# Kernel optimization log

Measured on AMD Instinct MI355X. Metric: run time of the kernel, lower is better.

The kernel has to match this reference:

```python
import jax, jax.numpy as jnp
import numpy as np

N = 100000   # nodes
E = 1600000  # edges
FEAT = 128
HID = 128
TGT = 64
L = 3
G = 512      # graphs in batch


def setup_inputs() -> dict:
    key = jax.random.key(0)
    ks = jax.random.split(key, 16)
    s = 0.05
    return {
        "x": jax.random.normal(ks[0], (N, FEAT), jnp.float32),
        "edge_index": jax.random.randint(ks[1], (2, E), 0, N, dtype=jnp.int32),
        "batch": jnp.sort(jax.random.randint(ks[2], (N,), 0, G, dtype=jnp.int32)),
        "conv_w1": jax.random.normal(ks[3], (L, FEAT, HID), jnp.float32) * s,
        "conv_b1": jax.random.normal(ks[4], (L, HID), jnp.float32) * s,
        "conv_w2": jax.random.normal(ks[5], (L, HID, HID), jnp.float32) * s,
        "conv_b2": jax.random.normal(ks[6], (L, HID), jnp.float32) * s,
        "eps": jnp.zeros((L,), jnp.float32),
        "gn_scale": jnp.ones((L, HID), jnp.float32),
        "gn_weight": jnp.ones((L, HID), jnp.float32),
        "gn_bias": jnp.zeros((L, HID), jnp.float32),
        "proj_w1": jax.random.normal(ks[7], (L, HID, HID), jnp.float32) * s,
        "proj_b1": jax.random.normal(ks[8], (L, HID), jnp.float32) * s,
        "proj_w2": jax.random.normal(ks[9], (L, HID, TGT), jnp.float32) * s,
        "proj_b2": jax.random.normal(ks[10], (L, TGT), jnp.float32) * s,
    }


def _graph_norm(h, batch, counts, scale, weight, bias):
    # per-graph mean -> scatter back to nodes
    mean = jax.ops.segment_sum(h, batch, num_segments=G) / counts
    sub = h - mean[batch] * scale
    var = jax.ops.segment_sum(sub * sub, batch, num_segments=G) / counts
    std = jnp.sqrt(var + 1e-8)
    return weight * sub / std[batch] + bias


def reference(x, edge_index, batch, conv_w1, conv_b1, conv_w2, conv_b2, eps,
              gn_scale, gn_weight, gn_bias, proj_w1, proj_b1, proj_w2, proj_b2):
    src, dst = edge_index[0], edge_index[1]
    counts = jnp.maximum(
        jax.ops.segment_sum(jnp.ones((N, 1), x.dtype), batch, num_segments=G), 1.0)
    h = x
    z_cat = []
    for l in range(L):
        # GINConv: aggr_j->i then 2-layer MLP
        aggr = jax.ops.segment_sum(h[src], dst, num_segments=N)
        h = (1.0 + eps[l]) * h + aggr
        h = jax.nn.relu(h @ conv_w1[l] + conv_b1[l]) @ conv_w2[l] + conv_b2[l]
        # GraphNorm
        h = _graph_norm(h, batch, counts, gn_scale[l], gn_weight[l], gn_bias[l])
        h = jax.nn.relu(h)
        # projection MLP + global add pool
        z = jax.nn.relu(h @ proj_w1[l] + proj_b1[l]) @ proj_w2[l] + proj_b2[l]
        z_cat.append(jax.ops.segment_sum(z, batch, num_segments=G))
    return jnp.concatenate(z_cat, axis=-1)  # [G, L*TGT]
```

## Files before the change

### kernel.cpp

```cpp
#include <hip/hip_runtime.h>

#define NN 100000
#define EE 1600000
#define HIDD 128
#define TGTT 64
#define GGG 512
#define NBK 98
#define CAPB 17408
#define ABLK 200
#define LSTR 136
#define CVTB 3125
#define GBLK 1563
#define FOUTB 128
#define OUTB 128

typedef unsigned short ushort_t;
typedef __attribute__((ext_vector_type(8))) short short8;
typedef __attribute__((ext_vector_type(4))) float f32x4;
typedef __attribute__((ext_vector_type(4))) unsigned short us4;

__device__ __forceinline__ float b2f(ushort_t u) {
    union { unsigned int i; float f; } v; v.i = ((unsigned int)u) << 16; return v.f;
}
__device__ __forceinline__ ushort_t f2b(float f) {
    union { float f; unsigned int i; } v; v.f = f;
    unsigned int r = (v.i + 0x7fffu + ((v.i >> 16) & 1u)) >> 16;
    return (ushort_t)r;
}

__global__ __launch_bounds__(256) void k_pro(const float* __restrict__ x, ushort_t* __restrict__ Xb,
                                             const float* __restrict__ cw1, const float* __restrict__ cw2,
                                             const float* __restrict__ pw1, ushort_t* __restrict__ Wt,
                                             const int* __restrict__ batch, int* __restrict__ goff,
                                             const int* __restrict__ ei, int* __restrict__ gcnt,
                                             unsigned int* __restrict__ bbuf) {
    __shared__ ushort_t sW[128 * 129];
    __shared__ int cnt[NBK], base[NBK], cur[NBK];
    int b = blockIdx.x, t = threadIdx.x;

    if (b < CVTB) {
        long i0 = (long)b * 1024 + t;
#pragma unroll
        for (int c = 0; c < 4; c++) {
            long i = i0 + c * 256;
            float4 v = ((const float4*)x)[i];
            us4 o; o.x = f2b(v.x); o.y = f2b(v.y); o.z = f2b(v.z); o.w = f2b(v.w);
            ((us4*)Xb)[i] = o;
        }
        return;
    }
    b -= CVTB;
    if (b < 9) {
        int l = b / 3, j = b % 3;
        const float* src = (j == 0 ? cw1 : j == 1 ? cw2 : pw1) + (size_t)l * HIDD * HIDD;
        ushort_t* dst = Wt + (size_t)b * HIDD * HIDD;
        for (int i = t; i < HIDD * HIDD; i += 256) {
            int k = i >> 7, n = i & 127;
            sW[n * 129 + k] = f2b(src[i]);
        }
        __syncthreads();
        for (int i = t; i < HIDD * HIDD; i += 256) {
            dst[i] = sW[(i >> 7) * 129 + (i & 127)];
        }
        return;
    }
    b -= 9;
    if (b < 3) {
        int g = b * 256 + t;
        if (g > GGG) return;
        int lo = 0, hi = NN;
        while (lo < hi) { int mid = (lo + hi) >> 1; if (batch[mid] < g) lo = mid + 1; else hi = mid; }
        goff[g] = lo;
        return;
    }
    b -= 3;
    {
        if (t < NBK) cnt[t] = 0;
        __syncthreads();
        int e0 = b * 8000;
        int e1 = min(e0 + 8000, EE);
        for (int e = e0 + t; e < e1; e += 256)
            atomicAdd(&cnt[ei[EE + e] >> 10], 1);
        __syncthreads();
        if (t < NBK) { base[t] = atomicAdd(&gcnt[t], cnt[t]); cur[t] = 0; }
        __syncthreads();
        for (int e = e0 + t; e < e1; e += 256) {
            int s = ei[e], d = ei[EE + e];
            int bk = d >> 10;
            int off = base[bk] + atomicAdd(&cur[bk], 1);
            if (off < CAPB)
                bbuf[(long)bk * CAPB + off] = (unsigned int)s | (((unsigned int)d & 1023u) << 17);
        }
    }
}

__global__ __launch_bounds__(256) void k_csr(const int* __restrict__ gcnt,
                                             const unsigned int* __restrict__ bbuf,
                                             int* __restrict__ rowptr, int* __restrict__ csr) {
    __shared__ int ldeg[1024], lcur[1024], tsum[256], sb[NBK];
    int b = blockIdx.x, t = threadIdx.x;
    if (t < NBK) sb[t] = gcnt[t];
    __syncthreads();
    if (t == 0) { int a = 0; for (int i = 0; i < NBK; i++) { int v = sb[i]; sb[i] = a; a += v; } }
    __syncthreads();
    int cnt = min(gcnt[b], CAPB);
    int base = sb[b];
    const unsigned int* bb = bbuf + (long)b * CAPB;
#pragma unroll
    for (int i = 0; i < 4; i++) ldeg[t + 256 * i] = 0;
    __syncthreads();
    for (int i = t; i < cnt; i += 256) atomicAdd(&ldeg[bb[i] >> 17], 1);
    __syncthreads();
    int d0 = ldeg[4 * t], d1 = ldeg[4 * t + 1], d2 = ldeg[4 * t + 2], d3 = ldeg[4 * t + 3];
    int tot = d0 + d1 + d2 + d3;
    tsum[t] = tot;
    __syncthreads();
    for (int off = 1; off < 256; off <<= 1) {
        int u = (t >= off) ? tsum[t - off] : 0;
        __syncthreads();
        tsum[t] += u;
        __syncthreads();
    }
    int texcl = tsum[t] - tot;
    int p0 = base + texcl, p1 = p0 + d0, p2 = p1 + d1, p3 = p2 + d2;
    lcur[4 * t] = p0; lcur[4 * t + 1] = p1; lcur[4 * t + 2] = p2; lcur[4 * t + 3] = p3;
    int gnode = b * 1024 + 4 * t;
    if (gnode < NN)     rowptr[gnode]     = p0;
    if (gnode + 1 < NN) rowptr[gnode + 1] = p1;
    if (gnode + 2 < NN) rowptr[gnode + 2] = p2;
    if (gnode + 3 < NN) rowptr[gnode + 3] = p3;
    if (b == NBK - 1 && t == 0) rowptr[NN] = EE;
    __syncthreads();
    for (int i = t; i < cnt; i += 256) {
        unsigned int en = bb[i];
        int pos = atomicAdd(&lcur[en >> 17], 1);
        csr[pos] = (int)(en & 0x1FFFFu);
    }
}

__global__ __launch_bounds__(256, 8) void k_gmlp(const ushort_t* __restrict__ hin,
                                              const int* __restrict__ rowptr,
                                              const int* __restrict__ csr,
                                              const float* __restrict__ eps, int l,
                                              const ushort_t* __restrict__ Wt1, const float* __restrict__ B1,
                                              const ushort_t* __restrict__ Wt2, const float* __restrict__ B2,
                                              ushort_t* __restrict__ Y,
                                              const float* __restrict__ pooledP, const int* __restrict__ goff,
                                              const float* __restrict__ WoP, const float* __restrict__ BoP,
                                              float* __restrict__ outP, int lprev) {
    __shared__ ushort_t sX[64 * LSTR];
    int tid = threadIdx.x;

    if (blockIdx.x >= GBLK) {
        if (lprev < 0) return;
        int ob = blockIdx.x - GBLK;
        int sub = tid >> 6, tt = tid & 63;
        int g = ob * 4 + sub;
        if (g >= GGG) return;
        float cntg = (float)(goff[g + 1] - goff[g]);
        float acc = cntg * BoP[tt];
        const float* p = pooledP + (long)g * HIDD;
        for (int k = 0; k < HIDD; k++) acc += p[k] * WoP[k * TGTT + tt];
        outP[(long)g * (3 * TGTT) + lprev * TGTT + tt] = acc;
        return;
    }

    long base = (long)blockIdx.x * 64;
    int lane = tid & 15, ng = tid >> 4;
    int off = lane << 3;
    float e1 = 1.0f + eps[l];

#pragma unroll 1
    for (int it = 0; it < 4; it++) {
        int row = it * 16 + ng;
        long node = base + row;
        short8 o = (short8)0;
        if (node < NN) {
            short8 h = *(const short8*)(hin + (node << 7) + off);
            float acc[8];
#pragma unroll
            for (int t = 0; t < 8; t++) acc[t] = e1 * b2f((ushort_t)h[t]);
            int jb = rowptr[node], je = rowptr[node + 1];
            int j = jb;
            for (; j + 8 <= je; j += 8) {
                int s0 = csr[j], s1 = csr[j + 1], s2 = csr[j + 2], s3 = csr[j + 3];
                int s4 = csr[j + 4], s5 = csr[j + 5], s6 = csr[j + 6], s7 = csr[j + 7];
                short8 v0 = *(const short8*)(hin + ((long)s0 << 7) + off);
                short8 v1 = *(const short8*)(hin + ((long)s1 << 7) + off);
                short8 v2 = *(const short8*)(hin + ((long)s2 << 7) + off);
                short8 v3 = *(const short8*)(hin + ((long)s3 << 7) + off);
                short8 v4 = *(const short8*)(hin + ((long)s4 << 7) + off);
                short8 v5 = *(const short8*)(hin + ((long)s5 << 7) + off);
                short8 v6 = *(const short8*)(hin + ((long)s6 << 7) + off);
                short8 v7 = *(const short8*)(hin + ((long)s7 << 7) + off);
#pragma unroll
                for (int t = 0; t < 8; t++)
                    acc[t] += ((b2f((ushort_t)v0[t]) + b2f((ushort_t)v1[t])) +
                               (b2f((ushort_t)v2[t]) + b2f((ushort_t)v3[t]))) +
                              ((b2f((ushort_t)v4[t]) + b2f((ushort_t)v5[t])) +
                               (b2f((ushort_t)v6[t]) + b2f((ushort_t)v7[t])));
            }
            for (; j + 4 <= je; j += 4) {
                int s0 = csr[j], s1 = csr[j + 1], s2 = csr[j + 2], s3 = csr[j + 3];
                short8 v0 = *(const short8*)(hin + ((long)s0 << 7) + off);
                short8 v1 = *(const short8*)(hin + ((long)s1 << 7) + off);
                short8 v2 = *(const short8*)(hin + ((long)s2 << 7) + off);
                short8 v3 = *(const short8*)(hin + ((long)s3 << 7) + off);
#pragma unroll
                for (int t = 0; t < 8; t++)
                    acc[t] += (b2f((ushort_t)v0[t]) + b2f((ushort_t)v1[t])) +
                              (b2f((ushort_t)v2[t]) + b2f((ushort_t)v3[t]));
            }
            for (; j < je; j++) {
                int s = csr[j];
                short8 v = *(const short8*)(hin + ((long)s << 7) + off);
#pragma unroll
                for (int t = 0; t < 8; t++) acc[t] += b2f((ushort_t)v[t]);
            }
#pragma unroll
            for (int t = 0; t < 8; t++) o[t] = (short)f2b(acc[t]);
        }
        *(short8*)(sX + row * LSTR + off) = o;
    }
    __syncthreads();

    int w = tid >> 6, l64 = tid & 63, q = l64 >> 4, l16 = l64 & 15;
    int r0 = w * 16;
    short8 a0[4];
#pragma unroll
    for (int c = 0; c < 4; c++)
        a0[c] = *(const short8*)(sX + (r0 + l16) * LSTR + q * 8 + c * 32);
    f32x4 acc0[8];
#pragma unroll
    for (int nt = 0; nt < 8; nt++) {
        int col = nt * 16 + l16;
        float bias = B1[col];
        f32x4 c0 = {bias, bias, bias, bias};
        const ushort_t* bB = Wt1 + col * HIDD + q * 8;
#pragma unroll
        for (int c = 0; c < 4; c++) {
            short8 b = *(const short8*)(bB + c * 32);
            c0 = __builtin_amdgcn_mfma_f32_16x16x32_bf16(a0[c], b, c0, 0, 0, 0);
        }
        acc0[nt] = c0;
    }
#pragma unroll
    for (int nt = 0; nt < 8; nt++) {
        int col = nt * 16 + l16;
#pragma unroll
        for (int r = 0; r < 4; r++)
            sX[(r0 + q * 4 + r) * LSTR + col] = f2b(fmaxf(acc0[nt][r], 0.f));
    }
#pragma unroll
    for (int c = 0; c < 4; c++)
        a0[c] = *(const short8*)(sX + (r0 + l16) * LSTR + q * 8 + c * 32);
#pragma unroll
    for (int nt = 0; nt < 8; nt++) {
        int col = nt * 16 + l16;
        float bias = B2[col];
        f32x4 c0 = {bias, bias, bias, bias};
        const ushort_t* bB = Wt2 + col * HIDD + q * 8;
#pragma unroll
        for (int c = 0; c < 4; c++) {
            short8 b = *(const short8*)(bB + c * 32);
            c0 = __builtin_amdgcn_mfma_f32_16x16x32_bf16(a0[c], b, c0, 0, 0, 0);
        }
#pragma unroll
        for (int r = 0; r < 4; r++) {
            long row0 = base + r0 + q * 4 + r;
            if (row0 < NN) Y[(row0 << 7) + col] = f2b(c0[r]);
        }
    }
}

__global__ __launch_bounds__(512) void k_gstat(const ushort_t* __restrict__ Hraw,
                                               const int* __restrict__ goff,
                                               const float* __restrict__ scale,
                                               const float* __restrict__ weight,
                                               float* __restrict__ msb, float* __restrict__ invb,
                                               float* __restrict__ pooled) {
    __shared__ float red[2][32][128];
    int g = blockIdx.x;
    int s = goff[g], e = goff[g + 1];
    float cnt = (float)max(e - s, 1);
    int lane = threadIdx.x & 15;
    int rg = threadIdx.x >> 4;
    int f0 = lane << 3;
    float sum[8], sq[8];
#pragma unroll
    for (int t = 0; t < 8; t++) { sum[t] = 0.f; sq[t] = 0.f; }
    for (int i = s + rg; i < e; i += 32) {
        short8 v = *(const short8*)(Hraw + ((long)i << 7) + f0);
#pragma unroll
        for (int t = 0; t < 8; t++) { float a = b2f((ushort_t)v[t]); sum[t] += a; sq[t] += a * a; }
    }
#pragma unroll
    for (int t = 0; t < 8; t++) { red[0][rg][f0 + t] = sum[t]; red[1][rg][f0 + t] = sq[t]; }
    __syncthreads();
    for (int off = 16; off > 0; off >>= 1) {
        if (rg < off) {
#pragma unroll
            for (int t = 0; t < 8; t++) {
                red[0][rg][f0 + t] += red[0][rg + off][f0 + t];
                red[1][rg][f0 + t] += red[1][rg + off][f0 + t];
            }
        }
        __syncthreads();
    }
    if (rg == 0) {
#pragma unroll
        for (int t = 0; t < 8; t++) {
            int f = f0 + t;
            float mean = red[0][0][f] / cnt;
            float ms = mean * scale[f];
            float var = red[1][0][f] / cnt - 2.f * ms * mean + ms * ms;
            msb[g * HIDD + f] = ms;
            invb[g * HIDD + f] = weight[f] / sqrtf(var + 1e-8f);
            pooled[g * HIDD + f] = 0.f;
        }
    }
}

__global__ __launch_bounds__(256, 8) void k_projpool(const ushort_t* __restrict__ Hraw,
                                                  const int* __restrict__ batch,
                                                  const float* __restrict__ msb, const float* __restrict__ invb,
                                                  const float* __restrict__ gnb,
                                                  const ushort_t* __restrict__ Wt, const float* __restrict__ B,
                                                  ushort_t* __restrict__ Hn, float* __restrict__ pooled,
                                                  int store_hn) {
    __shared__ ushort_t sX[64 * LSTR];
    __shared__ int sgid[64];
    int tid = threadIdx.x;
    long base = (long)blockIdx.x * 64;
#pragma unroll
    for (int c = 0; c < 4; c++) {
        int idx = c * 256 + tid;
        int row = idx >> 4, cw = idx & 15;
        long grow = base + row;
        short8 v = (short8)0;
        if (grow < NN) {
            short8 raw = *(const short8*)(Hraw + (grow << 7) + (cw << 3));
            int g = batch[grow];
            if (cw == 0) sgid[row] = g;
            const float* msp = msb + g * HIDD + (cw << 3);
            const float* ivp = invb + g * HIDD + (cw << 3);
            const float* gbp = gnb + (cw << 3);
            float4 m0 = *(const float4*)msp, m1 = *(const float4*)(msp + 4);
            float4 i0 = *(const float4*)ivp, i1 = *(const float4*)(ivp + 4);
            float4 g0 = *(const float4*)gbp, g1 = *(const float4*)(gbp + 4);
            float mv[8] = {m0.x, m0.y, m0.z, m0.w, m1.x, m1.y, m1.z, m1.w};
            float iv[8] = {i0.x, i0.y, i0.z, i0.w, i1.x, i1.y, i1.z, i1.w};
            float gv[8] = {g0.x, g0.y, g0.z, g0.w, g1.x, g1.y, g1.z, g1.w};
#pragma unroll
            for (int t = 0; t < 8; t++) {
                float val = (b2f((ushort_t)raw[t]) - mv[t]) * iv[t] + gv[t];
                v[t] = (short)f2b(val > 0.f ? val : 0.f);
            }
            if (store_hn) *(short8*)(Hn + (grow << 7) + (cw << 3)) = v;
        } else if (cw == 0) {
            sgid[row] = -1;
        }
        *(short8*)(sX + row * LSTR + (cw << 3)) = v;
    }
    __syncthreads();

    int w = tid >> 6, l64 = tid & 63, q = l64 >> 4, l16 = l64 & 15;
    int r0 = w * 16;
    short8 a0[4];
#pragma unroll
    for (int c = 0; c < 4; c++)
        a0[c] = *(const short8*)(sX + (r0 + l16) * LSTR + q * 8 + c * 32);
    f32x4 acc0[8];
#pragma unroll
    for (int nt = 0; nt < 8; nt++) {
        int col = nt * 16 + l16;
        float bias = B[col];
        f32x4 c0 = {bias, bias, bias, bias};
        const ushort_t* bB = Wt + col * HIDD + q * 8;
#pragma unroll
        for (int c = 0; c < 4; c++) {
            short8 b = *(const short8*)(bB + c * 32);
            c0 = __builtin_amdgcn_mfma_f32_16x16x32_bf16(a0[c], b, c0, 0, 0, 0);
        }
        acc0[nt] = c0;
    }
#pragma unroll
    for (int nt = 0; nt < 8; nt++) {
        int col = nt * 16 + l16;
#pragma unroll
        for (int r = 0; r < 4; r++)
            sX[(r0 + q * 4 + r) * LSTR + col] = f2b(fmaxf(acc0[nt][r], 0.f));
    }
    __syncthreads();

    int f = tid & 127, half = tid >> 7;
    int rbeg = half * 32, rend = rbeg + 32;
    float sum = 0.f;
    int curg = -1;
    for (int row = rbeg; row < rend; row++) {
        int g = sgid[row];
        if (g != curg) {
            if (curg >= 0) atomicAdd(&pooled[(long)curg * HIDD + f], sum);
            sum = 0.f; curg = g;
        }
        if (g >= 0) sum += b2f(sX[row * LSTR + f]);
    }
    if (curg >= 0) atomicAdd(&pooled[(long)curg * HIDD + f], sum);
}

__global__ __launch_bounds__(256) void k_out(const float* __restrict__ pooled, const int* __restrict__ goff,
                                             const float* __restrict__ W, const float* __restrict__ B,
                                             float* __restrict__ out, int l) {
    int sub = threadIdx.x >> 6, tt = threadIdx.x & 63;
    int g = blockIdx.x * 4 + sub;
    if (g >= GGG) return;
    float cnt = (float)(goff[g + 1] - goff[g]);
    float acc = cnt * B[tt];
    const float* p = pooled + (long)g * HIDD;
    for (int k = 0; k < HIDD; k++) acc += p[k] * W[k * TGTT + tt];
    out[(long)g * (3 * TGTT) + l * TGTT + tt] = acc;
}

extern "C" void kernel_launch(void* const* d_in, const int* in_sizes, int n_in,
                              void* d_out, int out_size, void* d_ws, size_t ws_size,
                              hipStream_t stream) {
    const float* x    = (const float*)d_in[0];
    const int*   ei   = (const int*)d_in[1];
    const int*   batch= (const int*)d_in[2];
    const float* cw1  = (const float*)d_in[3];
    const float* cb1  = (const float*)d_in[4];
    const float* cw2  = (const float*)d_in[5];
    const float* cb2  = (const float*)d_in[6];
    const float* eps  = (const float*)d_in[7];
    const float* gsc  = (const float*)d_in[8];
    const float* gw   = (const float*)d_in[9];
    const float* gb   = (const float*)d_in[10];
    const float* pw1  = (const float*)d_in[11];
    const float* pb1  = (const float*)d_in[12];
    const float* pw2  = (const float*)d_in[13];
    const float* pb2  = (const float*)d_in[14];
    float* out = (float*)d_out;

    ushort_t* Xb   = (ushort_t*)d_ws;
    ushort_t* Hn   = Xb;
    ushort_t* Hraw = Xb + (size_t)NN * HIDD;
    ushort_t* Wt   = Hraw + (size_t)NN * HIDD;
    float* msb     = (float*)(Wt + (size_t)9 * HIDD * HIDD);
    float* invb    = msb + (size_t)GGG * HIDD;
    float* pooled  = invb + (size_t)GGG * HIDD;
    int* goff   = (int*)(pooled + (size_t)GGG * HIDD);
    int* rowptr = goff + (GGG + 1);
    int* gcnt   = rowptr + (NN + 1);
    int* csr    = gcnt + NBK;
    unsigned int* bbuf = (unsigned int*)(csr + EE);

    hipMemsetAsync(gcnt, 0, NBK * sizeof(int), stream);
    k_pro<<<CVTB + 9 + 3 + ABLK, 256, 0, stream>>>(x, Xb, cw1, cw2, pw1, Wt, batch, goff, ei, gcnt, bbuf);
    k_csr<<<NBK, 256, 0, stream>>>(gcnt, bbuf, rowptr, csr);

    for (int l = 0; l < 3; l++) {
        const ushort_t* hin = (l == 0) ? Xb : Hn;
        ushort_t* Wt1 = Wt + (size_t)(l * 3 + 0) * HIDD * HIDD;
        ushort_t* Wt2 = Wt + (size_t)(l * 3 + 1) * HIDD * HIDD;
        ushort_t* Wtp = Wt + (size_t)(l * 3 + 2) * HIDD * HIDD;
        int grid = GBLK + (l > 0 ? FOUTB : 0);
        k_gmlp<<<grid, 256, 0, stream>>>(hin, rowptr, csr, eps, l,
                                         Wt1, cb1 + l * HIDD, Wt2, cb2 + l * HIDD, Hraw,
                                         pooled, goff,
                                         pw2 + (size_t)(l - 1) * HIDD * TGTT, pb2 + (l - 1) * TGTT,
                                         out, l - 1);
        k_gstat<<<GGG, 512, 0, stream>>>(Hraw, goff, gsc + l * HIDD, gw + l * HIDD, msb, invb, pooled);
        k_projpool<<<GBLK, 256, 0, stream>>>(Hraw, batch, msb, invb, gb + l * HIDD,
                                             Wtp, pb1 + l * HIDD, Hn, pooled, (l < 2) ? 1 : 0);
    }
    k_out<<<OUTB, 256, 0, stream>>>(pooled, goff, pw2 + (size_t)2 * HIDD * TGTT, pb2 + 2 * TGTT, out, 2);
}
```

Measured before the change: 676.4 us.

## Restructure preprocessing, CSR build, projection pooling, and output stage

After: 660.2 us. 1.02x faster.

```diff
diff --git a/kernel.cpp b/kernel.cpp
--- a/kernel.cpp
+++ b/kernel.cpp
@@ -7,12 +7,12 @@
 #define GGG 512
 #define NBK 98
 #define CAPB 17408
-#define ABLK 200
+#define ABLK 800
+#define EPB 2000
+#define CVT2 512
 #define LSTR 136
-#define CVTB 3125
-#define GBLK 1563
-#define FOUTB 128
-#define OUTB 128
+#define GBLKG 1563
+#define GBLKP 782
 
 typedef unsigned short ushort_t;
 typedef __attribute__((ext_vector_type(8))) short short8;
@@ -34,51 +34,14 @@
                                              const int* __restrict__ batch, int* __restrict__ goff,
                                              const int* __restrict__ ei, int* __restrict__ gcnt,
                                              unsigned int* __restrict__ bbuf) {
-    __shared__ ushort_t sW[128 * 129];
     __shared__ int cnt[NBK], base[NBK], cur[NBK];
     int b = blockIdx.x, t = threadIdx.x;
 
-    if (b < CVTB) {
-        long i0 = (long)b * 1024 + t;
-#pragma unroll
-        for (int c = 0; c < 4; c++) {
-            long i = i0 + c * 256;
-            float4 v = ((const float4*)x)[i];
-            us4 o; o.x = f2b(v.x); o.y = f2b(v.y); o.z = f2b(v.z); o.w = f2b(v.w);
-            ((us4*)Xb)[i] = o;
-        }
-        return;
-    }
-    b -= CVTB;
-    if (b < 9) {
-        int l = b / 3, j = b % 3;
-        const float* src = (j == 0 ? cw1 : j == 1 ? cw2 : pw1) + (size_t)l * HIDD * HIDD;
-        ushort_t* dst = Wt + (size_t)b * HIDD * HIDD;
-        for (int i = t; i < HIDD * HIDD; i += 256) {
-            int k = i >> 7, n = i & 127;
-            sW[n * 129 + k] = f2b(src[i]);
-        }
-        __syncthreads();
-        for (int i = t; i < HIDD * HIDD; i += 256) {
-            dst[i] = sW[(i >> 7) * 129 + (i & 127)];
-        }
-        return;
-    }
-    b -= 9;
-    if (b < 3) {
-        int g = b * 256 + t;
-        if (g > GGG) return;
-        int lo = 0, hi = NN;
-        while (lo < hi) { int mid = (lo + hi) >> 1; if (batch[mid] < g) lo = mid + 1; else hi = mid; }
-        goff[g] = lo;
-        return;
-    }
-    b -= 3;
-    {
+    if (b < ABLK) {
         if (t < NBK) cnt[t] = 0;
         __syncthreads();
-        int e0 = b * 8000;
-        int e1 = min(e0 + 8000, EE);
+        int e0 = b * EPB;
+        int e1 = min(e0 + EPB, EE);
         for (int e = e0 + t; e < e1; e += 256)
             atomicAdd(&cnt[ei[EE + e] >> 10], 1);
         __syncthreads();
@@ -91,80 +54,84 @@
             if (off < CAPB)
                 bbuf[(long)bk * CAPB + off] = (unsigned int)s | (((unsigned int)d & 1023u) << 17);
         }
-    }
-}
-
-__global__ __launch_bounds__(256) void k_csr(const int* __restrict__ gcnt,
-                                             const unsigned int* __restrict__ bbuf,
-                                             int* __restrict__ rowptr, int* __restrict__ csr) {
-    __shared__ int ldeg[1024], lcur[1024], tsum[256], sb[NBK];
+        return;
+    }
+    b -= ABLK;
+    if (b < CVT2) {
+        long total = (long)NN * HIDD / 4;
+        long step = (long)CVT2 * 256;
+        for (long i = (long)b * 256 + t; i < total; i += step) {
+            float4 v = ((const float4*)x)[i];
+            us4 o; o.x = f2b(v.x); o.y = f2b(v.y); o.z = f2b(v.z); o.w = f2b(v.w);
+            ((us4*)Xb)[i] = o;
+        }
+        return;
+    }
+    b -= CVT2;
+    if (b < 9) {
+        int l = b / 3, j = b % 3;
+        const float* src = (j == 0 ? cw1 : j == 1 ? cw2 : pw1) + (size_t)l * HIDD * HIDD;
+        ushort_t* dst = Wt + (size_t)b * HIDD * HIDD;
+        for (int i = t; i < HIDD * HIDD; i += 256)
+            dst[(i & 127) * HIDD + (i >> 7)] = f2b(src[i]);
+        return;
+    }
+    b -= 9;
+    {
+        int g = b * 256 + t;
+        if (g > GGG) return;
+        int lo = 0, hi = NN;
+        while (lo < hi) { int mid = (lo + hi) >> 1; if (batch[mid] < g) lo = mid + 1; else hi = mid; }
+        goff[g] = lo;
+    }
+}
+
+__global__ __launch_bounds__(1024) void k_csr(const int* __restrict__ gcnt,
+                                              const unsigned int* __restrict__ bbuf,
+                                              int* __restrict__ rowptr, int* __restrict__ csr) {
+    __shared__ int ldeg[1024], tsum[1024], sb[NBK];
     int b = blockIdx.x, t = threadIdx.x;
     if (t < NBK) sb[t] = gcnt[t];
+    ldeg[t] = 0;
     __syncthreads();
     if (t == 0) { int a = 0; for (int i = 0; i < NBK; i++) { int v = sb[i]; sb[i] = a; a += v; } }
     __syncthreads();
     int cnt = min(gcnt[b], CAPB);
     int base = sb[b];
     const unsigned int* bb = bbuf + (long)b * CAPB;
-#pragma unroll
-    for (int i = 0; i < 4; i++) ldeg[t + 256 * i] = 0;
-    __syncthreads();
-    for (int i = t; i < cnt; i += 256) atomicAdd(&ldeg[bb[i] >> 17], 1);
-    __syncthreads();
-    int d0 = ldeg[4 * t], d1 = ldeg[4 * t + 1], d2 = ldeg[4 * t + 2], d3 = ldeg[4 * t + 3];
-    int tot = d0 + d1 + d2 + d3;
-    tsum[t] = tot;
-    __syncthreads();
-    for (int off = 1; off < 256; off <<= 1) {
+    for (int i = t; i < cnt; i += 1024) atomicAdd(&ldeg[bb[i] >> 17], 1);
+    __syncthreads();
+    int d0 = ldeg[t];
+    tsum[t] = d0;
+    __syncthreads();
+    for (int off = 1; off < 1024; off <<= 1) {
         int u = (t >= off) ? tsum[t - off] : 0;
         __syncthreads();
         tsum[t] += u;
         __syncthreads();
     }
-    int texcl = tsum[t] - tot;
-    int p0 = base + texcl, p1 = p0 + d0, p2 = p1 + d1, p3 = p2 + d2;
-    lcur[4 * t] = p0; lcur[4 * t + 1] = p1; lcur[4 * t + 2] = p2; lcur[4 * t + 3] = p3;
-    int gnode = b * 1024 + 4 * t;
-    if (gnode < NN)     rowptr[gnode]     = p0;
-    if (gnode + 1 < NN) rowptr[gnode + 1] = p1;
-    if (gnode + 2 < NN) rowptr[gnode + 2] = p2;
-    if (gnode + 3 < NN) rowptr[gnode + 3] = p3;
+    int p0 = base + tsum[t] - d0;
+    int gnode = b * 1024 + t;
+    if (gnode < NN) rowptr[gnode] = p0;
     if (b == NBK - 1 && t == 0) rowptr[NN] = EE;
-    __syncthreads();
-    for (int i = t; i < cnt; i += 256) {
+    ldeg[t] = p0;
+    __syncthreads();
+    for (int i = t; i < cnt; i += 1024) {
         unsigned int en = bb[i];
-        int pos = atomicAdd(&lcur[en >> 17], 1);
+        int pos = atomicAdd(&ldeg[en >> 17], 1);
         csr[pos] = (int)(en & 0x1FFFFu);
     }
 }
 
-__global__ __launch_bounds__(256, 8) void k_gmlp(const ushort_t* __restrict__ hin,
+__global__ __launch_bounds__(256) void k_gmlp(const ushort_t* __restrict__ hin,
                                               const int* __restrict__ rowptr,
                                               const int* __restrict__ csr,
                                               const float* __restrict__ eps, int l,
                                               const ushort_t* __restrict__ Wt1, const float* __restrict__ B1,
                                               const ushort_t* __restrict__ Wt2, const float* __restrict__ B2,
-                                              ushort_t* __restrict__ Y,
-                                              const float* __restrict__ pooledP, const int* __restrict__ goff,
-                                              const float* __restrict__ WoP, const float* __restrict__ BoP,
-                                              float* __restrict__ outP, int lprev) {
+                                              ushort_t* __restrict__ Y) {
     __shared__ ushort_t sX[64 * LSTR];
     int tid = threadIdx.x;
-
-    if (blockIdx.x >= GBLK) {
-        if (lprev < 0) return;
-        int ob = blockIdx.x - GBLK;
-        int sub = tid >> 6, tt = tid & 63;
-        int g = ob * 4 + sub;
-        if (g >= GGG) return;
-        float cntg = (float)(goff[g + 1] - goff[g]);
-        float acc = cntg * BoP[tt];
-        const float* p = pooledP + (long)g * HIDD;
-        for (int k = 0; k < HIDD; k++) acc += p[k] * WoP[k * TGTT + tt];
-        outP[(long)g * (3 * TGTT) + lprev * TGTT + tt] = acc;
-        return;
-    }
-
     long base = (long)blockIdx.x * 64;
     int lane = tid & 15, ng = tid >> 4;
     int off = lane << 3;
@@ -266,10 +233,18 @@
             c0 = __builtin_amdgcn_mfma_f32_16x16x32_bf16(a0[c], b, c0, 0, 0, 0);
         }
 #pragma unroll
-        for (int r = 0; r < 4; r++) {
-            long row0 = base + r0 + q * 4 + r;
-            if (row0 < NN) Y[(row0 << 7) + col] = f2b(c0[r]);
-        }
+        for (int r = 0; r < 4; r++)
+            sX[(r0 + q * 4 + r) * LSTR + col] = f2b(c0[r]);
+    }
+    __syncthreads();
+
+#pragma unroll
+    for (int c = 0; c < 4; c++) {
+        int idx = c * 256 + tid;
+        int row = idx >> 4, cw = idx & 15;
+        long grow = base + row;
+        if (grow < NN)
+            *(short8*)(Y + (grow << 7) + (cw << 3)) = *(const short8*)(sX + row * LSTR + (cw << 3));
     }
 }
 
@@ -277,8 +252,7 @@
                                                const int* __restrict__ goff,
                                                const float* __restrict__ scale,
                                                const float* __restrict__ weight,
-                                               float* __restrict__ msb, float* __restrict__ invb,
-                                               float* __restrict__ pooled) {
+                                               float* __restrict__ msb, float* __restrict__ invb) {
     __shared__ float red[2][32][128];
     int g = blockIdx.x;
     int s = goff[g], e = goff[g + 1];
@@ -316,24 +290,23 @@
             float var = red[1][0][f] / cnt - 2.f * ms * mean + ms * ms;
             msb[g * HIDD + f] = ms;
             invb[g * HIDD + f] = weight[f] / sqrtf(var + 1e-8f);
-            pooled[g * HIDD + f] = 0.f;
-        }
-    }
-}
-
-__global__ __launch_bounds__(256, 8) void k_projpool(const ushort_t* __restrict__ Hraw,
+        }
+    }
+}
+
+__global__ __launch_bounds__(256) void k_projpool(const ushort_t* __restrict__ Hraw,
                                                   const int* __restrict__ batch,
                                                   const float* __restrict__ msb, const float* __restrict__ invb,
                                                   const float* __restrict__ gnb,
                                                   const ushort_t* __restrict__ Wt, const float* __restrict__ B,
-                                                  ushort_t* __restrict__ Hn, float* __restrict__ pooled,
+                                                  ushort_t* __restrict__ Hn, float* __restrict__ partial,
                                                   int store_hn) {
-    __shared__ ushort_t sX[64 * LSTR];
-    __shared__ int sgid[64];
+    __shared__ ushort_t sX[128 * LSTR];
+    __shared__ int sgid[128];
     int tid = threadIdx.x;
-    long base = (long)blockIdx.x * 64;
-#pragma unroll
-    for (int c = 0; c < 4; c++) {
+    long base = (long)blockIdx.x * 128;
+#pragma unroll
+    for (int c = 0; c < 8; c++) {
         int idx = c * 256 + tid;
         int row = idx >> 4, cw = idx & 15;
         long grow = base + row;
@@ -365,60 +338,88 @@
     __syncthreads();
 
     int w = tid >> 6, l64 = tid & 63, q = l64 >> 4, l16 = l64 & 15;
-    int r0 = w * 16;
-    short8 a0[4];
-#pragma unroll
-    for (int c = 0; c < 4; c++)
+    int r0 = w * 16, r1 = 64 + w * 16;
+    short8 a0[4], a1[4];
+#pragma unroll
+    for (int c = 0; c < 4; c++) {
         a0[c] = *(const short8*)(sX + (r0 + l16) * LSTR + q * 8 + c * 32);
-    f32x4 acc0[8];
+        a1[c] = *(const short8*)(sX + (r1 + l16) * LSTR + q * 8 + c * 32);
+    }
+    f32x4 acc0[8], acc1[8];
 #pragma unroll
     for (int nt = 0; nt < 8; nt++) {
         int col = nt * 16 + l16;
         float bias = B[col];
         f32x4 c0 = {bias, bias, bias, bias};
+        f32x4 c1 = c0;
         const ushort_t* bB = Wt + col * HIDD + q * 8;
 #pragma unroll
         for (int c = 0; c < 4; c++) {
             short8 b = *(const short8*)(bB + c * 32);
             c0 = __builtin_amdgcn_mfma_f32_16x16x32_bf16(a0[c], b, c0, 0, 0, 0);
-        }
-        acc0[nt] = c0;
+            c1 = __builtin_amdgcn_mfma_f32_16x16x32_bf16(a1[c], b, c1, 0, 0, 0);
+        }
+        acc0[nt] = c0; acc1[nt] = c1;
     }
 #pragma unroll
     for (int nt = 0; nt < 8; nt++) {
         int col = nt * 16 + l16;
 #pragma unroll
-        for (int r = 0; r < 4; r++)
+        for (int r = 0; r < 4; r++) {
             sX[(r0 + q * 4 + r) * LSTR + col] = f2b(fmaxf(acc0[nt][r], 0.f));
+            sX[(r1 + q * 4 + r) * LSTR + col] = f2b(fmaxf(acc1[nt][r], 0.f));
+        }
     }
     __syncthreads();
 
     int f = tid & 127, half = tid >> 7;
-    int rbeg = half * 32, rend = rbeg + 32;
+    int g0 = sgid[0];
+    long pbase = ((long)blockIdx.x * 4) * 2 + half;
+#pragma unroll
+    for (int s = 0; s < 4; s++)
+        partial[(pbase + (long)s * 2) * 128 + f] = 0.f;
+    int rbeg = half * 64, rend = rbeg + 64;
     float sum = 0.f;
     int curg = -1;
     for (int row = rbeg; row < rend; row++) {
         int g = sgid[row];
         if (g != curg) {
-            if (curg >= 0) atomicAdd(&pooled[(long)curg * HIDD + f], sum);
+            if (curg >= 0) partial[(pbase + (long)(curg - g0) * 2) * 128 + f] = sum;
             sum = 0.f; curg = g;
         }
         if (g >= 0) sum += b2f(sX[row * LSTR + f]);
     }
-    if (curg >= 0) atomicAdd(&pooled[(long)curg * HIDD + f], sum);
-}
-
-__global__ __launch_bounds__(256) void k_out(const float* __restrict__ pooled, const int* __restrict__ goff,
-                                             const float* __restrict__ W, const float* __restrict__ B,
-                                             float* __restrict__ out, int l) {
-    int sub = threadIdx.x >> 6, tt = threadIdx.x & 63;
-    int g = blockIdx.x * 4 + sub;
-    if (g >= GGG) return;
-    float cnt = (float)(goff[g + 1] - goff[g]);
-    float acc = cnt * B[tt];
-    const float* p = pooled + (long)g * HIDD;
-    for (int k = 0; k < HIDD; k++) acc += p[k] * W[k * TGTT + tt];
-    out[(long)g * (3 * TGTT) + l * TGTT + tt] = acc;
+    if (curg >= 0) partial[(pbase + (long)(curg - g0) * 2) * 128 + f] = sum;
+}
+
+__global__ __launch_bounds__(128) void k_poolred(const float* __restrict__ partial,
+                                                 const int* __restrict__ batch,
+                                                 const int* __restrict__ goff,
+                                                 const float* __restrict__ W, const float* __restrict__ B,
+                                                 float* __restrict__ out, int l) {
+    __shared__ float pv[128];
+    int g = blockIdx.x, f = threadIdx.x;
+    int s0 = goff[g], e0 = goff[g + 1];
+    float sum = 0.f;
+    if (e0 > s0) {
+        int bs = s0 >> 7, be = (e0 - 1) >> 7;
+        for (int b = bs; b <= be; b++) {
+            int g0 = batch[(long)b << 7];
+            int s = g - g0;
+            if (s >= 0 && s < 4) {
+                long pbase = ((long)b * 4 + s) * 2;
+                sum += partial[pbase * 128 + f] + partial[(pbase + 1) * 128 + f];
+            }
+        }
+    }
+    pv[f] = sum;
+    __syncthreads();
+    if (f < TGTT) {
+        float cnt = (float)(e0 - s0);
+        float acc = cnt * B[f];
+        for (int k = 0; k < HIDD; k++) acc += pv[k] * W[k * TGTT + f];
+        out[(long)g * (3 * TGTT) + l * TGTT + f] = acc;
+    }
 }
 
 extern "C" void kernel_launch(void* const* d_in, const int* in_sizes, int n_in,
@@ -447,31 +448,29 @@
     ushort_t* Wt   = Hraw + (size_t)NN * HIDD;
     float* msb     = (float*)(Wt + (size_t)9 * HIDD * HIDD);
     float* invb    = msb + (size_t)GGG * HIDD;
-    float* pooled  = invb + (size_t)GGG * HIDD;
-    int* goff   = (int*)(pooled + (size_t)GGG * HIDD);
+    float* pooled_unused = invb + (size_t)GGG * HIDD;
+    int* goff   = (int*)(pooled_unused + (size_t)GGG * HIDD);
     int* rowptr = goff + (GGG + 1);
     int* gcnt   = rowptr + (NN + 1);
     int* csr    = gcnt + NBK;
     unsigned int* bbuf = (unsigned int*)(csr + EE);
+    float* partial = (float*)bbuf;
 
     hipMemsetAsync(gcnt, 0, NBK * sizeof(int), stream);
-    k_pro<<<CVTB + 9 + 3 + ABLK, 256, 0, stream>>>(x, Xb, cw1, cw2, pw1, Wt, batch, goff, ei, gcnt, bbuf);
-    k_csr<<<NBK, 256, 0, stream>>>(gcnt, bbuf, rowptr, csr);
+    k_pro<<<ABLK + CVT2 + 9 + 3, 256, 0, stream>>>(x, Xb, cw1, cw2, pw1, Wt, batch, goff, ei, gcnt, bbuf);
+    k_csr<<<NBK, 1024, 0, stream>>>(gcnt, bbuf, rowptr, csr);
 
     for (int l = 0; l < 3; l++) {
         const ushort_t* hin = (l == 0) ? Xb : Hn;
         ushort_t* Wt1 = Wt + (size_t)(l * 3 + 0) * HIDD * HIDD;
         ushort_t* Wt2 = Wt + (size_t)(l * 3 + 1) * HIDD * HIDD;
         ushort_t* Wtp = Wt + (size_t)(l * 3 + 2) * HIDD * HIDD;
-        int grid = GBLK + (l > 0 ? FOUTB : 0);
-        k_gmlp<<<grid, 256, 0, stream>>>(hin, rowptr, csr, eps, l,
-                                         Wt1, cb1 + l * HIDD, Wt2, cb2 + l * HIDD, Hraw,
-                                         pooled, goff,
-                                         pw2 + (size_t)(l - 1) * HIDD * TGTT, pb2 + (l - 1) * TGTT,
-                                         out, l - 1);
-        k_gstat<<<GGG, 512, 0, stream>>>(Hraw, goff, gsc + l * HIDD, gw + l * HIDD, msb, invb, pooled);
-        k_projpool<<<GBLK, 256, 0, stream>>>(Hraw, batch, msb, invb, gb + l * HIDD,
-                                             Wtp, pb1 + l * HIDD, Hn, pooled, (l < 2) ? 1 : 0);
-    }
-    k_out<<<OUTB, 256, 0, stream>>>(pooled, goff, pw2 + (size_t)2 * HIDD * TGTT, pb2 + 2 * TGTT, out, 2);
-}
+        k_gmlp<<<GBLKG, 256, 0, stream>>>(hin, rowptr, csr, eps, l,
+                                          Wt1, cb1 + l * HIDD, Wt2, cb2 + l * HIDD, Hraw);
+        k_gstat<<<GGG, 512, 0, stream>>>(Hraw, goff, gsc + l * HIDD, gw + l * HIDD, msb, invb);
+        k_projpool<<<GBLKP, 256, 0, stream>>>(Hraw, batch, msb, invb, gb + l * HIDD,
+                                              Wtp, pb1 + l * HIDD, Hn, partial, (l < 2) ? 1 : 0);
+        k_poolred<<<GGG, 128, 0, stream>>>(partial, batch, goff,
+                                           pw2 + (size_t)l * HIDD * TGTT, pb2 + l * TGTT, out, l);
+    }
+}
```
